# Kernel optimization log

Hardware: AMD Instinct MI355X
Metric: run time of the kernel (lower is better)

## Reference

```python
import jax, jax.numpy as jnp
import numpy as np

BATCH, DIM = 8192, 1024  # batch of ODE states, state dimension (orig dim=100 scaled up)
ETA = 1.0                # self.eta
B_DECAY = 1.0            # self.B (linear decay coefficient)


def setup_inputs() -> dict:
    key = jax.random.key(0)
    k1, k2, k3, k4, k5 = jax.random.split(key, 5)
    return {
        "x":      jax.random.normal(k1, (BATCH, DIM), jnp.float32),
        "e_x":    jax.random.normal(k2, (BATCH, DIM), jnp.float32),
        "W":      jax.random.normal(k3, (BATCH, DIM), jnp.float32),
        "A":      jax.random.normal(k4, (DIM, DIM), jnpp := jnp.float32) / np.float32(np.sqrt(DIM)),
        "target": jax.random.normal(k5, (1, DIM), jnp.float32),
    }


def reference(x, e_x, W, A, target):
    # b_ast = diagonal of B_ast = diag(target^2 / (1 + target^2)); mm with a diag
    # matrix == elementwise multiply by its diagonal.  [1, D]
    b_ast = target ** 2 / (1.0 + target ** 2)
    # control: u = -eta * (W * (x + e_x - target)) @ B_ast              [B, D]
    u = -ETA * (W * ((x + e_x) - target)) * b_ast
    # saturating nonlinearity sigma(x) = x^2 / (1 + x^2)                [B, D]
    sig = x ** 2 / (1.0 + x ** 2)
    # dx = -B*x + A @ sigma(x) (per state: sigma(x) @ A^T) + u*sigma(x) [B, D]
    dx = -B_DECAY * x + sig @ A.T + u * sig
    # original returns tuple(dx_i) + tuple(-dx_i) + tuple(zeros): stack as [3, B, D]
    return jnp.stack([dx, -dx, jnp.zeros_like(dx)])
```

## Files before the change

kernel.cpp:

```cpp
#include <hip/hip_runtime.h>
#include <hip/hip_bf16.h>
#include <stdint.h>

#define BATCH 8192
#define DIM   1024
#define BM 64
#define BN 64
#define BK 64
#define NT (DIM / BK)

typedef __attribute__((ext_vector_type(4))) float f32x4;
typedef __attribute__((ext_vector_type(8))) short bf16x8;
typedef __attribute__((ext_vector_type(4))) unsigned short u16x4;
typedef __attribute__((ext_vector_type(8))) unsigned short u16x8;

#define AS1(p) ((const __attribute__((address_space(1))) void*)(p))
#define AS3(p) ((__attribute__((address_space(3))) void*)(p))

__device__ __forceinline__ unsigned short f2bf(float f) {
    union { __hip_bfloat16 h; unsigned short u; } v;
    v.h = __hip_bfloat16(f);
    return v.u;
}

__device__ __forceinline__ float sigma_f(float x) {
    float x2 = x * x;
    return x2 * __builtin_amdgcn_rcpf(1.0f + x2);
}

__global__ __launch_bounds__(256) void convA_kernel(
    const float* __restrict__ A, unsigned short* __restrict__ Ab)
{
    int idx = blockIdx.x * 256 + threadIdx.x;
    f32x4 av = ((const f32x4*)A)[idx];
    u16x4 ab;
#pragma unroll
    for (int i = 0; i < 4; ++i) ab[i] = f2bf(av[i]);
    ((u16x4*)Ab)[idx] = ab;
}

__global__ __launch_bounds__(256, 5) void fused_kernel(
    const float* __restrict__ x, const float* __restrict__ ex,
    const float* __restrict__ W, const float* __restrict__ tgt,
    const unsigned short* __restrict__ Ab,
    float* __restrict__ out0, float* __restrict__ out1,
    float* __restrict__ out2)
{
    __shared__ __align__(16) char lds[32768];

    const int b     = blockIdx.x;
    const int xcd   = b & 7;
    const int local = b >> 3;
    const int bm    = xcd * 16 + (local >> 4);
    const int bn    = local & 15;

    const int tid  = threadIdx.x;
    const int lane = tid & 63;
    const int wid  = tid >> 6;
    const int wr   = wid >> 1;
    const int wc   = wid & 1;
    const int l15  = lane & 15;

    const int swz = (((lane & 7) ^ (lane >> 3)) << 4);
    const char* gBb = (const char*)Ab +
        ((size_t)(bn * BN + wid * 16 + (lane >> 3)) * DIM) * 2 + swz;

    const int r0 = tid >> 3;
    const int g  = tid & 7;
    const float* gx = x + (size_t)(bm * BM + r0) * DIM + g * 8;
    const int wAoff = (g * 16) ^ ((r0 & 7) << 4);

    const int rd_sw = (lane & 7) << 4;
    const int cb0   = (lane >> 4) << 4;

    f32x4 acc[2][2];
#pragma unroll
    for (int mi = 0; mi < 2; ++mi)
#pragma unroll
        for (int ni = 0; ni < 2; ++ni)
            acc[mi][ni] = f32x4{0.f, 0.f, 0.f, 0.f};

    auto stageB = [&](int k, char* Bs) {
#pragma unroll
        for (int j = 0; j < 2; ++j)
            __builtin_amdgcn_global_load_lds(
                AS1(gBb + (size_t)j * (8 * DIM * 2) + (size_t)k * 2),
                AS3(Bs + (wid * 16 + j * 8) * 128), 16, 0, 0);
    };
    auto loadX = [&](int k, f32x4 xa[2][2]) {
#pragma unroll
        for (int s = 0; s < 2; ++s) {
            xa[s][0] = *(const f32x4*)(gx + (size_t)s * 32 * DIM + k);
            xa[s][1] = *(const f32x4*)(gx + (size_t)s * 32 * DIM + k + 4);
        }
    };
    auto writeSig = [&](char* As, f32x4 xa[2][2]) {
#pragma unroll
        for (int s = 0; s < 2; ++s) {
            u16x8 sb;
#pragma unroll
            for (int i = 0; i < 4; ++i) {
                sb[i]     = f2bf(sigma_f(xa[s][0][i]));
                sb[i + 4] = f2bf(sigma_f(xa[s][1][i]));
            }
            *(u16x8*)(As + (r0 + s * 32) * 128 + wAoff) = sb;
        }
    };

    {
        f32x4 xa[2][2];
        loadX(0, xa);
        stageB(0, lds + 8192);
        writeSig(lds, xa);
    }
    __syncthreads();

    for (int t = 0; t < NT; ++t) {
        const int cur = t & 1;
        f32x4 xa[2][2];
        if (t + 1 < NT) {
            loadX((t + 1) * BK, xa);
            stageB((t + 1) * BK, lds + (cur ^ 1) * 16384 + 8192);
        }
        __builtin_amdgcn_sched_barrier(0);

        const char* As_ = lds + cur * 16384;
        const char* Bs_ = As_ + 8192;
#pragma unroll
        for (int kk = 0; kk < 2; ++kk) {
            bf16x8 af[2], bfr[2];
#pragma unroll
            for (int mi = 0; mi < 2; ++mi)
                af[mi] = *(const bf16x8*)(As_ + (wr * 32 + mi * 16 + l15) * 128 +
                                          ((cb0 + kk * 64) ^ rd_sw));
#pragma unroll
            for (int ni = 0; ni < 2; ++ni)
                bfr[ni] = *(const bf16x8*)(Bs_ + (wc * 32 + ni * 16 + l15) * 128 +
                                           ((cb0 + kk * 64) ^ rd_sw));
#pragma unroll
            for (int mi = 0; mi < 2; ++mi)
#pragma unroll
                for (int ni = 0; ni < 2; ++ni)
                    acc[mi][ni] = __builtin_amdgcn_mfma_f32_16x16x32_bf16(
                        af[mi], bfr[ni], acc[mi][ni], 0, 0, 0);
        }
        __builtin_amdgcn_sched_barrier(0);

        if (t + 1 < NT) writeSig(lds + (cur ^ 1) * 16384, xa);
        __syncthreads();
    }

#pragma unroll
    for (int mi = 0; mi < 2; ++mi)
#pragma unroll
        for (int ni = 0; ni < 2; ++ni) {
            const int row_ = wr * 32 + mi * 16 + ((lane >> 4) << 2);
            const int colb = (wc * 32 + ni * 16 + l15) * 4;
#pragma unroll
            for (int r = 0; r < 4; ++r)
                *(float*)(lds + (row_ + r) * 256 + colb) = acc[mi][ni][r];
        }
    __syncthreads();

#pragma unroll
    for (int p = 0; p < 4; ++p) {
        const int ci  = tid + p * 256;
        const int row = ci >> 4;
        const int cv  = ci & 15;
        f32x4 c = *(const f32x4*)(lds + row * 256 + cv * 16);
        const size_t v4 = (size_t)(bm * BM + row) * (DIM / 4) + bn * (BN / 4) + cv;
        f32x4 xv = ((const f32x4*)x)[v4];
        f32x4 ev = ((const f32x4*)ex)[v4];
        f32x4 wv = ((const f32x4*)W)[v4];
        f32x4 tv = ((const f32x4*)tgt)[bn * (BN / 4) + cv];
        f32x4 o0;
#pragma unroll
        for (int e = 0; e < 4; ++e) {
            float xi = xv[e], ti = tv[e];
            float ba = ti * ti * __builtin_amdgcn_rcpf(1.0f + ti * ti);
            float u  = -(wv[e] * (xi + ev[e] - ti)) * ba;
            float s  = sigma_f(xi);
            o0[e] = -xi + u * s + c[e];
        }
        ((f32x4*)out0)[v4] = o0;
        ((f32x4*)out1)[v4] = -o0;
        ((f32x4*)out2)[v4] = f32x4{0.f, 0.f, 0.f, 0.f};
    }
}

extern "C" void kernel_launch(void* const* d_in, const int* in_sizes, int n_in,
                              void* d_out, int out_size, void* d_ws, size_t ws_size,
                              hipStream_t stream)
{
    const float* x   = (const float*)d_in[0];
    const float* ex  = (const float*)d_in[1];
    const float* W   = (const float*)d_in[2];
    const float* A   = (const float*)d_in[3];
    const float* tgt = (const float*)d_in[4];

    float* out0 = (float*)d_out;
    float* out1 = out0 + (size_t)BATCH * DIM;
    float* out2 = out1 + (size_t)BATCH * DIM;

    unsigned short* Abf = (unsigned short*)d_ws;

    convA_kernel<<<DIM * DIM / 4 / 256, 256, 0, stream>>>(A, Abf);
    fused_kernel<<<(BATCH / BM) * (DIM / BN), 256, 0, stream>>>(
        x, ex, W, tgt, Abf, out0, out1, out2);
}
```

Measured before the change: 65.63 us.

## Precompute sigma(x) in bf16 and use triple-buffered direct-to-LDS GEMM with 128-row tiles

```diff
diff --git a/kernel.cpp b/kernel.cpp
--- a/kernel.cpp
+++ b/kernel.cpp
@@ -4,14 +4,14 @@
 
 #define BATCH 8192
 #define DIM   1024
-#define BM 64
+#define BM 128
 #define BN 64
 #define BK 64
-#define NT (DIM / BK)
+#define STEPS 16
+#define BUF 24576
 
 typedef __attribute__((ext_vector_type(4))) float f32x4;
 typedef __attribute__((ext_vector_type(8))) short bf16x8;
-typedef __attribute__((ext_vector_type(4))) unsigned short u16x4;
 typedef __attribute__((ext_vector_type(8))) unsigned short u16x8;
 
 #define AS1(p) ((const __attribute__((address_space(1))) void*)(p))
@@ -22,139 +22,135 @@
     v.h = __hip_bfloat16(f);
     return v.u;
 }
-
 __device__ __forceinline__ float sigma_f(float x) {
     float x2 = x * x;
     return x2 * __builtin_amdgcn_rcpf(1.0f + x2);
 }
 
-__global__ __launch_bounds__(256) void convA_kernel(
-    const float* __restrict__ A, unsigned short* __restrict__ Ab)
+__global__ __launch_bounds__(256) void prep_kernel(
+    const float* __restrict__ x, const float* __restrict__ A,
+    unsigned short* __restrict__ sigb, unsigned short* __restrict__ Abf)
 {
-    int idx = blockIdx.x * 256 + threadIdx.x;
-    f32x4 av = ((const f32x4*)A)[idx];
-    u16x4 ab;
-#pragma unroll
-    for (int i = 0; i < 4; ++i) ab[i] = f2bf(av[i]);
-    ((u16x4*)Ab)[idx] = ab;
-}
-
-__global__ __launch_bounds__(256, 5) void fused_kernel(
+    const int i = blockIdx.x * 256 + threadIdx.x;
+    if (i < BATCH * DIM / 8) {
+        f32x4 v0 = ((const f32x4*)x)[i * 2];
+        f32x4 v1 = ((const f32x4*)x)[i * 2 + 1];
+        u16x8 sb;
+#pragma unroll
+        for (int e = 0; e < 4; ++e) {
+            sb[e]     = f2bf(sigma_f(v0[e]));
+            sb[e + 4] = f2bf(sigma_f(v1[e]));
+        }
+        ((u16x8*)sigb)[i] = sb;
+    } else {
+        const int j = i - BATCH * DIM / 8;
+        f32x4 v0 = ((const f32x4*)A)[j * 2];
+        f32x4 v1 = ((const f32x4*)A)[j * 2 + 1];
+        u16x8 ab;
+#pragma unroll
+        for (int e = 0; e < 4; ++e) {
+            ab[e]     = f2bf(v0[e]);
+            ab[e + 4] = f2bf(v1[e]);
+        }
+        ((u16x8*)Abf)[j] = ab;
+    }
+}
+
+__global__ __launch_bounds__(256, 2) void gemm_kernel(
     const float* __restrict__ x, const float* __restrict__ ex,
     const float* __restrict__ W, const float* __restrict__ tgt,
-    const unsigned short* __restrict__ Ab,
+    const unsigned short* __restrict__ sigb,
+    const unsigned short* __restrict__ Abf,
     float* __restrict__ out0, float* __restrict__ out1,
     float* __restrict__ out2)
 {
-    __shared__ __align__(16) char lds[32768];
+    __shared__ __align__(16) char lds[3 * BUF];
 
     const int b     = blockIdx.x;
     const int xcd   = b & 7;
     const int local = b >> 3;
-    const int bm    = xcd * 16 + (local >> 4);
+    const int bm    = xcd * 8 + (local >> 4);
     const int bn    = local & 15;
 
     const int tid  = threadIdx.x;
     const int lane = tid & 63;
     const int wid  = tid >> 6;
-    const int wr   = wid >> 1;
-    const int wc   = wid & 1;
+    const int wr   = wid >> 1, wc = wid & 1;
     const int l15  = lane & 15;
 
     const int swz = (((lane & 7) ^ (lane >> 3)) << 4);
-    const char* gBb = (const char*)Ab +
-        ((size_t)(bn * BN + wid * 16 + (lane >> 3)) * DIM) * 2 + swz;
-
-    const int r0 = tid >> 3;
-    const int g  = tid & 7;
-    const float* gx = x + (size_t)(bm * BM + r0) * DIM + g * 8;
-    const int wAoff = (g * 16) ^ ((r0 & 7) << 4);
+    const char* gS = (const char*)sigb +
+        ((size_t)(bm * BM + wid * 8 + (lane >> 3)) * DIM) * 2 + swz;
+    const char* gB = (const char*)Abf +
+        ((size_t)(bn * BN + wid * 8 + (lane >> 3)) * DIM) * 2 + swz;
 
     const int rd_sw = (lane & 7) << 4;
     const int cb0   = (lane >> 4) << 4;
 
-    f32x4 acc[2][2];
-#pragma unroll
-    for (int mi = 0; mi < 2; ++mi)
+    f32x4 acc[4][2];
+#pragma unroll
+    for (int mi = 0; mi < 4; ++mi)
 #pragma unroll
         for (int ni = 0; ni < 2; ++ni)
             acc[mi][ni] = f32x4{0.f, 0.f, 0.f, 0.f};
 
-    auto stageB = [&](int k, char* Bs) {
+    auto stage = [&](int t) {
+        char* As = lds + (t % 3) * BUF;
+        char* Bs = As + 16384;
+        const size_t ko = (size_t)t * (BK * 2);
+#pragma unroll
+        for (int j = 0; j < 4; ++j)
+            __builtin_amdgcn_global_load_lds(
+                AS1(gS + (size_t)j * (32 * DIM * 2) + ko),
+                AS3(As + (wid * 8 + j * 32) * 128), 16, 0, 0);
 #pragma unroll
         for (int j = 0; j < 2; ++j)
             __builtin_amdgcn_global_load_lds(
-                AS1(gBb + (size_t)j * (8 * DIM * 2) + (size_t)k * 2),
-                AS3(Bs + (wid * 16 + j * 8) * 128), 16, 0, 0);
+                AS1(gB + (size_t)j * (32 * DIM * 2) + ko),
+                AS3(Bs + (wid * 8 + j * 32) * 128), 16, 0, 0);
     };
-    auto loadX = [&](int k, f32x4 xa[2][2]) {
-#pragma unroll
-        for (int s = 0; s < 2; ++s) {
-            xa[s][0] = *(const f32x4*)(gx + (size_t)s * 32 * DIM + k);
-            xa[s][1] = *(const f32x4*)(gx + (size_t)s * 32 * DIM + k + 4);
-        }
-    };
-    auto writeSig = [&](char* As, f32x4 xa[2][2]) {
-#pragma unroll
-        for (int s = 0; s < 2; ++s) {
-            u16x8 sb;
-#pragma unroll
-            for (int i = 0; i < 4; ++i) {
-                sb[i]     = f2bf(sigma_f(xa[s][0][i]));
-                sb[i + 4] = f2bf(sigma_f(xa[s][1][i]));
-            }
-            *(u16x8*)(As + (r0 + s * 32) * 128 + wAoff) = sb;
-        }
-    };
-
-    {
-        f32x4 xa[2][2];
-        loadX(0, xa);
-        stageB(0, lds + 8192);
-        writeSig(lds, xa);
-    }
-    __syncthreads();
-
-    for (int t = 0; t < NT; ++t) {
-        const int cur = t & 1;
-        f32x4 xa[2][2];
-        if (t + 1 < NT) {
-            loadX((t + 1) * BK, xa);
-            stageB((t + 1) * BK, lds + (cur ^ 1) * 16384 + 8192);
-        }
-        __builtin_amdgcn_sched_barrier(0);
-
-        const char* As_ = lds + cur * 16384;
-        const char* Bs_ = As_ + 8192;
+
+    stage(0);
+    stage(1);
+
+    for (int t = 0; t < STEPS; ++t) {
+        __builtin_amdgcn_sched_barrier(0);
+        if (t < STEPS - 1) asm volatile("s_waitcnt vmcnt(6)" ::: "memory");
+        else               asm volatile("s_waitcnt vmcnt(0)" ::: "memory");
+        __builtin_amdgcn_sched_barrier(0);
+        __builtin_amdgcn_s_barrier();
+        __builtin_amdgcn_sched_barrier(0);
+        if (t + 2 < STEPS) stage(t + 2);
+        __builtin_amdgcn_sched_barrier(0);
+
+        const char* As_ = lds + (t % 3) * BUF;
+        const char* Bs_ = As_ + 16384;
 #pragma unroll
         for (int kk = 0; kk < 2; ++kk) {
-            bf16x8 af[2], bfr[2];
-#pragma unroll
-            for (int mi = 0; mi < 2; ++mi)
-                af[mi] = *(const bf16x8*)(As_ + (wr * 32 + mi * 16 + l15) * 128 +
+            bf16x8 af[4], bfr[2];
+#pragma unroll
+            for (int mi = 0; mi < 4; ++mi)
+                af[mi] = *(const bf16x8*)(As_ + (wr * 64 + mi * 16 + l15) * 128 +
                                           ((cb0 + kk * 64) ^ rd_sw));
 #pragma unroll
             for (int ni = 0; ni < 2; ++ni)
                 bfr[ni] = *(const bf16x8*)(Bs_ + (wc * 32 + ni * 16 + l15) * 128 +
                                            ((cb0 + kk * 64) ^ rd_sw));
 #pragma unroll
-            for (int mi = 0; mi < 2; ++mi)
+            for (int mi = 0; mi < 4; ++mi)
 #pragma unroll
                 for (int ni = 0; ni < 2; ++ni)
                     acc[mi][ni] = __builtin_amdgcn_mfma_f32_16x16x32_bf16(
                         af[mi], bfr[ni], acc[mi][ni], 0, 0, 0);
         }
-        __builtin_amdgcn_sched_barrier(0);
-
-        if (t + 1 < NT) writeSig(lds + (cur ^ 1) * 16384, xa);
-        __syncthreads();
     }
 
-#pragma unroll
-    for (int mi = 0; mi < 2; ++mi)
+    __syncthreads();
+#pragma unroll
+    for (int mi = 0; mi < 4; ++mi)
 #pragma unroll
         for (int ni = 0; ni < 2; ++ni) {
-            const int row_ = wr * 32 + mi * 16 + ((lane >> 4) << 2);
+            const int row_ = wr * 64 + mi * 16 + ((lane >> 4) << 2);
             const int colb = (wc * 32 + ni * 16 + l15) * 4;
 #pragma unroll
             for (int r = 0; r < 4; ++r)
@@ -163,16 +159,16 @@
     __syncthreads();
 
 #pragma unroll
-    for (int p = 0; p < 4; ++p) {
-        const int ci  = tid + p * 256;
+    for (int p = 0; p < 8; ++p) {
+        const int ci  = p * 256 + tid;
         const int row = ci >> 4;
         const int cv  = ci & 15;
         f32x4 c = *(const f32x4*)(lds + row * 256 + cv * 16);
-        const size_t v4 = (size_t)(bm * BM + row) * (DIM / 4) + bn * (BN / 4) + cv;
+        const size_t v4 = (size_t)(bm * BM + row) * (DIM / 4) + bn * 16 + cv;
         f32x4 xv = ((const f32x4*)x)[v4];
         f32x4 ev = ((const f32x4*)ex)[v4];
         f32x4 wv = ((const f32x4*)W)[v4];
-        f32x4 tv = ((const f32x4*)tgt)[bn * (BN / 4) + cv];
+        f32x4 tv = ((const f32x4*)tgt)[bn * 16 + cv];
         f32x4 o0;
 #pragma unroll
         for (int e = 0; e < 4; ++e) {
@@ -202,9 +198,10 @@
     float* out1 = out0 + (size_t)BATCH * DIM;
     float* out2 = out1 + (size_t)BATCH * DIM;
 
-    unsigned short* Abf = (unsigned short*)d_ws;
-
-    convA_kernel<<<DIM * DIM / 4 / 256, 256, 0, stream>>>(A, Abf);
-    fused_kernel<<<(BATCH / BM) * (DIM / BN), 256, 0, stream>>>(
-        x, ex, W, tgt, Abf, out0, out1, out2);
-}
+    unsigned short* sigb = (unsigned short*)d_ws;
+    unsigned short* Abf  = (unsigned short*)((char*)d_ws + (size_t)16 * 1024 * 1024);
+
+    prep_kernel<<<4608, 256, 0, stream>>>(x, A, sigb, Abf);
+    gemm_kernel<<<(BATCH / BM) * (DIM / BN), 256, 0, stream>>>(
+        x, ex, W, tgt, sigb, Abf, out0, out1, out2);
+}
```

After: 55.71 us. -15.1%, faster.
